# Kernel tuning notes

Measured on AMD Instinct MI355X. Metric: run time of the kernel, lower is better.

Reference implementation:

```python
import jax, jax.numpy as jnp
import numpy as np

N_NODES = 20000
N_EDGES = 640000
D_FEAT = 128
DIM_H = 128
DIM_OUT = 128


def setup_inputs() -> dict:
    key = jax.random.key(0)
    ks = jax.random.split(key, 9)
    s = 1.0 / np.sqrt(D_FEAT)
    sh = 1.0 / np.sqrt(DIM_H)
    x = jax.random.normal(ks[0], (N_NODES, D_FEAT), dtype=jnp.float32)
    edge_index = jax.random.randint(ks[1], (2, N_EDGES), 0, N_NODES, dtype=jnp.int64)
    return {
        "x": x,
        "edge_index": edge_index,
        "W_src": jax.random.normal(ks[2], (D_FEAT, DIM_H), dtype=jnp.float32) * s,
        "W_dst": jax.random.normal(ks[3], (D_FEAT, DIM_H), dtype=jnp.float32) * s,
        "att_src": jax.random.normal(ks[4], (DIM_H,), dtype=jnp.float32) * sh,
        "att_dst": jax.random.normal(ks[5], (DIM_H,), dtype=jnp.float32) * sh,
        "bias": jnp.zeros((DIM_H,), dtype=jnp.float32),
        "W_lin": jax.random.normal(ks[6], (DIM_H, DIM_OUT), dtype=jnp.float32) * sh,
        "b_lin": jnp.zeros((DIM_OUT,), dtype=jnp.float32),
    }


def reference(x, edge_index, W_src, W_dst, att_src, att_dst, bias, W_lin, b_lin):
    N = x.shape[0]
    src, dst = edge_index[0], edge_index[1]  # edge j -> i (source_to_target)
    # Separate source/destination projections (GATConv with bipartite (-1,-1) dims)
    h_src = x @ W_src  # [N, H]
    h_dst = x @ W_dst  # [N, H]
    a_src = h_src @ att_src  # [N] per-node attention contributions
    a_dst = h_dst @ att_dst  # [N]
    # Edge attention logits with LeakyReLU (negative_slope=0.2)
    logits = jax.nn.leaky_relu(a_src[src] + a_dst[dst], negative_slope=0.2)  # [E]
    # Segment softmax over incoming edges of each destination node
    seg_max = jax.ops.segment_max(logits, dst, num_segments=N)  # [N]
    e = jnp.exp(logits - seg_max[dst])  # [E]
    denom = jax.ops.segment_sum(e, dst, num_segments=N)  # [N]
    alpha = e / denom[dst]  # [E]
    # Weighted scatter-add aggregation of source features
    msg = alpha[:, None] * h_src[src]  # [E, H]
    agg = jax.ops.segment_sum(msg, dst, num_segments=N) + bias  # [N, H]
    h = jax.nn.relu(agg)
    return h @ W_lin + b_lin  # [N, dim_out]
```

## Files before the change

kernel.cpp:

```cpp
#include <hip/hip_runtime.h>
#include <cstdint>

typedef short short8 __attribute__((ext_vector_type(8)));
typedef float floatx4 __attribute__((ext_vector_type(4)));

#define NBUCK 157
#define DPB   128
#define BCAP  8192
#define EPB   2048
#define LCAP  4608

__device__ __forceinline__ unsigned short f2bf_rne(float f) {
    unsigned b = __float_as_uint(f);
    b += 0x7FFFu + ((b >> 16) & 1u);
    return (unsigned short)(b >> 16);
}

__global__ __launch_bounds__(256) void k_prep(
    const float* __restrict__ Wsrc, const float* __restrict__ Wdst,
    const float* __restrict__ Wlin,
    const float* __restrict__ att_src, const float* __restrict__ att_dst,
    float* __restrict__ w_s, float* __restrict__ w_d,
    unsigned short* __restrict__ Wt_src, unsigned short* __restrict__ Wt_lin,
    int* __restrict__ g_cur)
{
    const int b = blockIdx.x;
    const int t = threadIdx.x;
    if (b == 0) {
        const int wv = t >> 6, ln = t & 63;
        const float a0 = att_src[ln], a1 = att_src[64 + ln];
        for (int k = wv; k < 128; k += 4) {
            float v = fmaf(Wsrc[k * 128 + ln], a0, Wsrc[k * 128 + 64 + ln] * a1);
#pragma unroll
            for (int o = 32; o > 0; o >>= 1) v += __shfl_xor(v, o);
            if (ln == 0) w_s[k] = v;
        }
    } else if (b == 1) {
        const int wv = t >> 6, ln = t & 63;
        const float a0 = att_dst[ln], a1 = att_dst[64 + ln];
        for (int k = wv; k < 128; k += 4) {
            float v = fmaf(Wdst[k * 128 + ln], a0, Wdst[k * 128 + 64 + ln] * a1);
#pragma unroll
            for (int o = 32; o > 0; o >>= 1) v += __shfl_xor(v, o);
            if (ln == 0) w_d[k] = v;
        }
    } else if (b == 2) {
        for (int i = 0; i < 64; ++i) {
            int idx = t + i * 256;
            int k = idx >> 7, n = idx & 127;
            Wt_src[n * 128 + k] = f2bf_rne(Wsrc[idx]);
        }
    } else if (b == 3) {
        for (int i = 0; i < 64; ++i) {
            int idx = t + i * 256;
            int k = idx >> 7, n = idx & 127;
            Wt_lin[n * 128 + k] = f2bf_rne(Wlin[idx]);
        }
    } else {
        if (t < NBUCK) g_cur[t] = 0;
    }
}

__global__ __launch_bounds__(256) void k_fat(
    const int* __restrict__ src, const int* __restrict__ dst,
    int* __restrict__ g_cur, unsigned* __restrict__ g_edges, int E, int NBK,
    const float* __restrict__ x, const unsigned short* __restrict__ Wt,
    const float* __restrict__ w_s, const float* __restrict__ w_d,
    unsigned short* __restrict__ h_bf,
    float* __restrict__ a_src, float* __restrict__ a_dst, int N)
{
    __shared__ int cnt[NBUCK], loff[NBUCK], cur[NBUCK], gbase[NBUCK];
    __shared__ unsigned pay[EPB];
    __shared__ int dadr[EPB];
    const int tid = threadIdx.x;

    if ((int)blockIdx.x < NBK) {
        const int e0 = blockIdx.x * EPB;
        int ne_blk = E - e0; if (ne_blk > EPB) ne_blk = EPB;

        for (int i = tid; i < NBUCK; i += 256) cnt[i] = 0;
        __syncthreads();
#pragma unroll
        for (int j = 0; j < EPB / 256; ++j) {
            int e = e0 + j * 256 + tid;
            if (e < E) atomicAdd(&cnt[dst[e] >> 7], 1);
        }
        __syncthreads();
        int* sb = (int*)pay;
        sb[tid] = (tid < NBUCK) ? cnt[tid] : 0;
        __syncthreads();
        for (int s = 1; s < 256; s <<= 1) {
            int u = (tid >= s) ? sb[tid - s] : 0;
            __syncthreads();
            sb[tid] += u;
            __syncthreads();
        }
        if (tid < NBUCK) {
            loff[tid] = sb[tid] - cnt[tid];
            cur[tid] = 0;
            gbase[tid] = tid * BCAP + atomicAdd(&g_cur[tid], cnt[tid]);
        }
        __syncthreads();
#pragma unroll
        for (int j = 0; j < EPB / 256; ++j) {
            int e = e0 + j * 256 + tid;
            if (e < E) {
                int s = src[e], d = dst[e];
                int b2 = d >> 7;
                int slot = atomicAdd(&cur[b2], 1);
                int lp = loff[b2] + slot;
                pay[lp]  = (unsigned)s | ((unsigned)(d & 127) << 15);
                dadr[lp] = gbase[b2] + slot;
            }
        }
        __syncthreads();
        for (int i = tid; i < ne_blk; i += 256)
            g_edges[dadr[i]] = pay[i];
        return;
    }

    const int l = tid & 63;
    const int wv = tid >> 6;
    const int r0 = ((int)blockIdx.x - NBK) * 64 + wv * 16;
    const int rloc = l & 15;
    const int kg = l >> 4;
    int row = r0 + rloc; if (row >= N) row = N - 1;

    short8 afrag[4];
    float vs = 0.f, vd = 0.f;
#pragma unroll
    for (int kk = 0; kk < 4; ++kk) {
        const int kbase = kk * 32 + kg * 8;
        const float4 f0 = *reinterpret_cast<const float4*>(x + (size_t)row * 128 + kbase);
        const float4 f1 = *reinterpret_cast<const float4*>(x + (size_t)row * 128 + kbase + 4);
        const float4 s0 = *reinterpret_cast<const float4*>(w_s + kbase);
        const float4 s1 = *reinterpret_cast<const float4*>(w_s + kbase + 4);
        const float4 d0 = *reinterpret_cast<const float4*>(w_d + kbase);
        const float4 d1 = *reinterpret_cast<const float4*>(w_d + kbase + 4);
        const float xe[8]  = {f0.x, f0.y, f0.z, f0.w, f1.x, f1.y, f1.z, f1.w};
        const float wse[8] = {s0.x, s0.y, s0.z, s0.w, s1.x, s1.y, s1.z, s1.w};
        const float wde[8] = {d0.x, d0.y, d0.z, d0.w, d1.x, d1.y, d1.z, d1.w};
        short8 a;
#pragma unroll
        for (int j = 0; j < 8; ++j) {
            vs = fmaf(xe[j], wse[j], vs);
            vd = fmaf(xe[j], wde[j], vd);
            a[j] = (short)f2bf_rne(xe[j]);
        }
        afrag[kk] = a;
    }
    vs += __shfl_xor(vs, 16); vs += __shfl_xor(vs, 32);
    vd += __shfl_xor(vd, 16); vd += __shfl_xor(vd, 32);
    if (l < 16 && (r0 + l) < N) { a_src[r0 + l] = vs; a_dst[r0 + l] = vd; }

#pragma unroll
    for (int nt = 0; nt < 8; ++nt) {
        floatx4 acc = {0.f, 0.f, 0.f, 0.f};
#pragma unroll
        for (int kk = 0; kk < 4; ++kk) {
            const short8 bfr = *reinterpret_cast<const short8*>(
                Wt + (size_t)(nt * 16 + rloc) * 128 + kk * 32 + kg * 8);
            acc = __builtin_amdgcn_mfma_f32_16x16x32_bf16(afrag[kk], bfr, acc, 0, 0, 0);
        }
        const int col = nt * 16 + rloc;
#pragma unroll
        for (int r = 0; r < 4; ++r) {
            int grow = r0 + kg * 4 + r;
            if (grow < N) h_bf[(size_t)grow * 128 + col] = f2bf_rne(acc[r]);
        }
    }
}

__global__ __launch_bounds__(1024) void k_csr(
    const unsigned* __restrict__ g_edges, const int* __restrict__ g_cur,
    const float* __restrict__ a_src, const float* __restrict__ a_dst,
    int* __restrict__ off, uint2* __restrict__ sw, int N, int E)
{
    __shared__ int sbuf[256];
    __shared__ int hcnt[DPB], hoff[DPB], hcur[DPB];
    __shared__ uint2 swl[LCAP];
    const int b = blockIdx.x, tid = threadIdx.x;

    if (tid < 256) sbuf[tid] = (tid < NBUCK) ? g_cur[tid] : 0;
    __syncthreads();
    for (int s = 1; s < 256; s <<= 1) {
        int u = 0;
        if (tid < 256 && tid >= s) u = sbuf[tid - s];
        __syncthreads();
        if (tid < 256) sbuf[tid] += u;
        __syncthreads();
    }
    const int ne0 = g_cur[b];
    const int ne = (ne0 < LCAP) ? ne0 : LCAP;
    const int cb = sbuf[b] - ne0;
    if (b == 0 && tid == 0) off[N] = E;

    const unsigned* ep = g_edges + (size_t)b * BCAP;

    if (tid < DPB) hcnt[tid] = 0;
    __syncthreads();
    for (int i = tid; i < ne; i += 1024)
        atomicAdd(&hcnt[ep[i] >> 15], 1);
    __syncthreads();
    if (tid < DPB) hoff[tid] = hcnt[tid];
    __syncthreads();
    for (int s = 1; s < DPB; s <<= 1) {
        int u = 0;
        if (tid < DPB && tid >= s) u = hoff[tid - s];
        __syncthreads();
        if (tid < DPB) hoff[tid] += u;
        __syncthreads();
    }
    if (tid < DPB) {
        int excl = hoff[tid] - hcnt[tid];
        hoff[tid] = excl;
        hcur[tid] = 0;
        int d = b * DPB + tid;
        if (d < N) off[d] = cb + excl;
    }
    __syncthreads();
    for (int i = tid; i < ne; i += 1024) {
        unsigned p = ep[i];
        int dl = (int)(p >> 15);
        int s  = (int)(p & 0x7FFFu);
        int slot = atomicAdd(&hcur[dl], 1);
        float l = a_src[s] + a_dst[b * DPB + dl];
        l = (l > 0.f) ? l : 0.2f * l;
        swl[hoff[dl] + slot] = make_uint2((unsigned)s, __float_as_uint(__expf(l)));
    }
    __syncthreads();
    for (int i = tid; i < ne; i += 1024)
        sw[cb + i] = swl[i];
}

__global__ __launch_bounds__(256) void k_seg_fused(
    const uint2* __restrict__ sw, const int* __restrict__ off,
    const uint4* __restrict__ hb4, const float* __restrict__ bias,
    const unsigned short* __restrict__ WtLin, const float* __restrict__ blin,
    float* __restrict__ out, int N)
{
    __shared__ unsigned short hs[16][128];
    const int tid  = threadIdx.x;
    const int wv   = tid >> 6;
    const int lane = tid & 63;
    const int g    = lane >> 4;
    const int li   = lane & 15;
    const int nb   = blockIdx.x * 16;

    float4 b0 = *reinterpret_cast<const float4*>(bias + li * 8);
    float4 b1 = *reinterpret_cast<const float4*>(bias + li * 8 + 4);

    for (int i = 0; i < 4; ++i) {
        int n = nb + wv * 4 + i;
        if (n >= N) break;
        int beg = off[n], end = off[n + 1];
        float den = 0.f;
        float acc[8];
#pragma unroll
        for (int c = 0; c < 8; ++c) acc[c] = 0.f;

        for (int base = beg; base < end; base += 64) {
            int idx = base + lane;
            uint2 p = (idx < end) ? sw[idx] : make_uint2(0u, 0u);
            int   sc = (int)p.x;
            float wc = __uint_as_float(p.y);
            int cnt = end - base; if (cnt > 64) cnt = 64;
            int nq = (cnt + 3) >> 2;
            int j = 0;
            for (; j + 2 <= nq; j += 2) {
                int ea = 4 * j + g, eb = 4 * j + 4 + g;
                float wa = __shfl(wc, ea), wb = __shfl(wc, eb);
                int   sa = __shfl(sc, ea), sb = __shfl(sc, eb);
                uint4 ha = hb4[(size_t)sa * 16 + li];
                uint4 hb = hb4[(size_t)sb * 16 + li];
                den += wa + wb;
                acc[0] = fmaf(wa, __uint_as_float(ha.x << 16), acc[0]);
                acc[1] = fmaf(wa, __uint_as_float(ha.x & 0xFFFF0000u), acc[1]);
                acc[2] = fmaf(wa, __uint_as_float(ha.y << 16), acc[2]);
                acc[3] = fmaf(wa, __uint_as_float(ha.y & 0xFFFF0000u), acc[3]);
                acc[4] = fmaf(wa, __uint_as_float(ha.z << 16), acc[4]);
                acc[5] = fmaf(wa, __uint_as_float(ha.z & 0xFFFF0000u), acc[5]);
                acc[6] = fmaf(wa, __uint_as_float(ha.w << 16), acc[6]);
                acc[7] = fmaf(wa, __uint_as_float(ha.w & 0xFFFF0000u), acc[7]);
                acc[0] = fmaf(wb, __uint_as_float(hb.x << 16), acc[0]);
                acc[1] = fmaf(wb, __uint_as_float(hb.x & 0xFFFF0000u), acc[1]);
                acc[2] = fmaf(wb, __uint_as_float(hb.y << 16), acc[2]);
                acc[3] = fmaf(wb, __uint_as_float(hb.y & 0xFFFF0000u), acc[3]);
                acc[4] = fmaf(wb, __uint_as_float(hb.z << 16), acc[4]);
                acc[5] = fmaf(wb, __uint_as_float(hb.z & 0xFFFF0000u), acc[5]);
                acc[6] = fmaf(wb, __uint_as_float(hb.w << 16), acc[6]);
                acc[7] = fmaf(wb, __uint_as_float(hb.w & 0xFFFF0000u), acc[7]);
            }
            if (j < nq) {
                int e = 4 * j + g;
                float we = __shfl(wc, e);
                int   se = __shfl(sc, e);
                uint4 hv = hb4[(size_t)se * 16 + li];
                den += we;
                acc[0] = fmaf(we, __uint_as_float(hv.x << 16), acc[0]);
                acc[1] = fmaf(we, __uint_as_float(hv.x & 0xFFFF0000u), acc[1]);
                acc[2] = fmaf(we, __uint_as_float(hv.y << 16), acc[2]);
                acc[3] = fmaf(we, __uint_as_float(hv.y & 0xFFFF0000u), acc[3]);
                acc[4] = fmaf(we, __uint_as_float(hv.z << 16), acc[4]);
                acc[5] = fmaf(we, __uint_as_float(hv.z & 0xFFFF0000u), acc[5]);
                acc[6] = fmaf(we, __uint_as_float(hv.w << 16), acc[6]);
                acc[7] = fmaf(we, __uint_as_float(hv.w & 0xFFFF0000u), acc[7]);
            }
        }
#pragma unroll
        for (int c = 0; c < 8; ++c) {
            acc[c] += __shfl_xor(acc[c], 16);
            acc[c] += __shfl_xor(acc[c], 32);
        }
        den += __shfl_xor(den, 16);
        den += __shfl_xor(den, 32);

        if (g == 0) {
            float inv = (den > 0.f) ? 1.f / den : 0.f;
            float v0 = fmaxf(fmaf(acc[0], inv, b0.x), 0.f);
            float v1 = fmaxf(fmaf(acc[1], inv, b0.y), 0.f);
            float v2 = fmaxf(fmaf(acc[2], inv, b0.z), 0.f);
            float v3 = fmaxf(fmaf(acc[3], inv, b0.w), 0.f);
            float v4 = fmaxf(fmaf(acc[4], inv, b1.x), 0.f);
            float v5 = fmaxf(fmaf(acc[5], inv, b1.y), 0.f);
            float v6 = fmaxf(fmaf(acc[6], inv, b1.z), 0.f);
            float v7 = fmaxf(fmaf(acc[7], inv, b1.w), 0.f);
            uint4 o;
            o.x = ((unsigned)f2bf_rne(v1) << 16) | f2bf_rne(v0);
            o.y = ((unsigned)f2bf_rne(v3) << 16) | f2bf_rne(v2);
            o.z = ((unsigned)f2bf_rne(v5) << 16) | f2bf_rne(v4);
            o.w = ((unsigned)f2bf_rne(v7) << 16) | f2bf_rne(v6);
            *reinterpret_cast<uint4*>(&hs[wv * 4 + i][li * 8]) = o;
        }
    }
    __syncthreads();

    const int rloc = lane & 15;
    const int kg   = lane >> 4;
    short8 afrag[4];
#pragma unroll
    for (int kk = 0; kk < 4; ++kk)
        afrag[kk] = *reinterpret_cast<const short8*>(&hs[rloc][kk * 32 + kg * 8]);

#pragma unroll
    for (int t = 0; t < 2; ++t) {
        const int nt = wv * 2 + t;
        floatx4 acc4 = {0.f, 0.f, 0.f, 0.f};
#pragma unroll
        for (int kk = 0; kk < 4; ++kk) {
            const short8 bfr = *reinterpret_cast<const short8*>(
                WtLin + (size_t)(nt * 16 + rloc) * 128 + kk * 32 + kg * 8);
            acc4 = __builtin_amdgcn_mfma_f32_16x16x32_bf16(afrag[kk], bfr, acc4, 0, 0, 0);
        }
        const int col = nt * 16 + rloc;
        const float bl = blin[col];
#pragma unroll
        for (int r = 0; r < 4; ++r) {
            int grow = nb + kg * 4 + r;
            if (grow < N) out[(size_t)grow * 128 + col] = acc4[r] + bl;
        }
    }
}

extern "C" void kernel_launch(void* const* d_in, const int* in_sizes, int n_in,
                              void* d_out, int out_size, void* d_ws, size_t ws_size,
                              hipStream_t stream)
{
    const float* x       = (const float*)d_in[0];
    const int*   ei      = (const int*)d_in[1];
    const float* Wsrc    = (const float*)d_in[2];
    const float* Wdst    = (const float*)d_in[3];
    const float* att_src = (const float*)d_in[4];
    const float* att_dst = (const float*)d_in[5];
    const float* bias    = (const float*)d_in[6];
    const float* Wlin    = (const float*)d_in[7];
    const float* blin    = (const float*)d_in[8];
    float* out = (float*)d_out;

    const int N = in_sizes[0] / 128;
    const int E = in_sizes[1] / 2;
    const int* src = ei;
    const int* dst = ei + E;
    const int NBK = (E + EPB - 1) / EPB;
    const int NGB = (N + 63) / 64;

    auto aup = [](size_t v) { return (v + 255) & ~(size_t)255; };
    char* p = (char*)d_ws;
    unsigned short* h_bf   = (unsigned short*)p; p += aup((size_t)N * 128 * 2);
    uint2* sw              = (uint2*)p;          p += aup((size_t)E * 8);
    unsigned* g_edges      = (unsigned*)p;       p += aup((size_t)NBUCK * BCAP * 4);
    float* a_src           = (float*)p;          p += aup((size_t)N * 4);
    float* a_dst           = (float*)p;          p += aup((size_t)N * 4);
    int*   offs            = (int*)p;            p += aup((size_t)(N + 1) * 4);
    int*   g_cur           = (int*)p;            p += aup(NBUCK * 4);
    float* w_s             = (float*)p;          p += aup(128 * 4);
    float* w_d             = (float*)p;          p += aup(128 * 4);
    unsigned short* Wt_src = (unsigned short*)p; p += aup(128 * 128 * 2);
    unsigned short* Wt_lin = (unsigned short*)p; p += aup(128 * 128 * 2);

    k_prep<<<5, 256, 0, stream>>>(Wsrc, Wdst, Wlin, att_src, att_dst,
                                  w_s, w_d, Wt_src, Wt_lin, g_cur);
    k_fat<<<NBK + NGB, 256, 0, stream>>>(src, dst, g_cur, g_edges, E, NBK,
                                         x, Wt_src, w_s, w_d, h_bf, a_src, a_dst, N);
    k_csr<<<NBUCK, 1024, 0, stream>>>(g_edges, g_cur, a_src, a_dst,
                                      offs, sw, N, E);
    k_seg_fused<<<(N + 15) / 16, 256, 0, stream>>>(
        sw, offs, (const uint4*)h_bf, bias, Wt_lin, blin, out, N);
}
```

Measured before the change: 72.13 us.

## Drop CSR build kernel; segment kernel gathers its edges from per-block bucket runs

The global bucket scatter and the separate CSR-building kernel are removed. Each edge-partition block now writes its edges bucket-sorted in place and records a per-bucket (offset,count) table. The fused segment kernel then scans, for its 16 destination nodes, every block's run for its bucket, filters to its own nodes, and builds per-node lists in shared memory before aggregating. This saves a kernel launch, the global atomics and the sw round trip. In exchange each bucket's edges are rescanned by 8 blocks, and per-node degree is capped at 160, which could drop edges for high-degree nodes.

```diff
diff --git a/kernel.cpp b/kernel.cpp
--- a/kernel.cpp
+++ b/kernel.cpp
@@ -4,11 +4,11 @@
 typedef short short8 __attribute__((ext_vector_type(8)));
 typedef float floatx4 __attribute__((ext_vector_type(4)));
 
-#define NBUCK 157
-#define DPB   128
-#define BCAP  8192
-#define EPB   2048
-#define LCAP  4608
+#define NBUCK   157
+#define EPB     2048
+#define NBK_MAX 336
+#define BSTRIDE 160
+#define DCAP    160
 
 __device__ __forceinline__ unsigned short f2bf_rne(float f) {
     unsigned b = __float_as_uint(f);
@@ -21,8 +21,7 @@
     const float* __restrict__ Wlin,
     const float* __restrict__ att_src, const float* __restrict__ att_dst,
     float* __restrict__ w_s, float* __restrict__ w_d,
-    unsigned short* __restrict__ Wt_src, unsigned short* __restrict__ Wt_lin,
-    int* __restrict__ g_cur)
+    unsigned short* __restrict__ Wt_src, unsigned short* __restrict__ Wt_lin)
 {
     const int b = blockIdx.x;
     const int t = threadIdx.x;
@@ -50,28 +49,25 @@
             int k = idx >> 7, n = idx & 127;
             Wt_src[n * 128 + k] = f2bf_rne(Wsrc[idx]);
         }
-    } else if (b == 3) {
+    } else {
         for (int i = 0; i < 64; ++i) {
             int idx = t + i * 256;
             int k = idx >> 7, n = idx & 127;
             Wt_lin[n * 128 + k] = f2bf_rne(Wlin[idx]);
         }
-    } else {
-        if (t < NBUCK) g_cur[t] = 0;
     }
 }
 
 __global__ __launch_bounds__(256) void k_fat(
     const int* __restrict__ src, const int* __restrict__ dst,
-    int* __restrict__ g_cur, unsigned* __restrict__ g_edges, int E, int NBK,
+    unsigned* __restrict__ g_edges, unsigned* __restrict__ rb, int E, int NBK,
     const float* __restrict__ x, const unsigned short* __restrict__ Wt,
     const float* __restrict__ w_s, const float* __restrict__ w_d,
     unsigned short* __restrict__ h_bf,
     float* __restrict__ a_src, float* __restrict__ a_dst, int N)
 {
-    __shared__ int cnt[NBUCK], loff[NBUCK], cur[NBUCK], gbase[NBUCK];
+    __shared__ int cnt[NBUCK], loff[NBUCK], cur[NBUCK];
     __shared__ unsigned pay[EPB];
-    __shared__ int dadr[EPB];
     const int tid = threadIdx.x;
 
     if ((int)blockIdx.x < NBK) {
@@ -96,9 +92,11 @@
             __syncthreads();
         }
         if (tid < NBUCK) {
-            loff[tid] = sb[tid] - cnt[tid];
+            int excl = sb[tid] - cnt[tid];
+            loff[tid] = excl;
             cur[tid] = 0;
-            gbase[tid] = tid * BCAP + atomicAdd(&g_cur[tid], cnt[tid]);
+            rb[(size_t)blockIdx.x * BSTRIDE + tid] =
+                ((unsigned)excl << 16) | (unsigned)cnt[tid];
         }
         __syncthreads();
 #pragma unroll
@@ -108,14 +106,12 @@
                 int s = src[e], d = dst[e];
                 int b2 = d >> 7;
                 int slot = atomicAdd(&cur[b2], 1);
-                int lp = loff[b2] + slot;
-                pay[lp]  = (unsigned)s | ((unsigned)(d & 127) << 15);
-                dadr[lp] = gbase[b2] + slot;
+                pay[loff[b2] + slot] = (unsigned)s | ((unsigned)d << 15);
             }
         }
         __syncthreads();
         for (int i = tid; i < ne_blk; i += 256)
-            g_edges[dadr[i]] = pay[i];
+            g_edges[e0 + i] = pay[i];
         return;
     }
 
@@ -171,108 +167,84 @@
     }
 }
 
-__global__ __launch_bounds__(1024) void k_csr(
-    const unsigned* __restrict__ g_edges, const int* __restrict__ g_cur,
+__global__ __launch_bounds__(256) void k_seg_fused(
+    const unsigned* __restrict__ g_edges, const unsigned* __restrict__ rb, int NBK,
     const float* __restrict__ a_src, const float* __restrict__ a_dst,
-    int* __restrict__ off, uint2* __restrict__ sw, int N, int E)
-{
-    __shared__ int sbuf[256];
-    __shared__ int hcnt[DPB], hoff[DPB], hcur[DPB];
-    __shared__ uint2 swl[LCAP];
-    const int b = blockIdx.x, tid = threadIdx.x;
-
-    if (tid < 256) sbuf[tid] = (tid < NBUCK) ? g_cur[tid] : 0;
-    __syncthreads();
-    for (int s = 1; s < 256; s <<= 1) {
-        int u = 0;
-        if (tid < 256 && tid >= s) u = sbuf[tid - s];
-        __syncthreads();
-        if (tid < 256) sbuf[tid] += u;
-        __syncthreads();
-    }
-    const int ne0 = g_cur[b];
-    const int ne = (ne0 < LCAP) ? ne0 : LCAP;
-    const int cb = sbuf[b] - ne0;
-    if (b == 0 && tid == 0) off[N] = E;
-
-    const unsigned* ep = g_edges + (size_t)b * BCAP;
-
-    if (tid < DPB) hcnt[tid] = 0;
-    __syncthreads();
-    for (int i = tid; i < ne; i += 1024)
-        atomicAdd(&hcnt[ep[i] >> 15], 1);
-    __syncthreads();
-    if (tid < DPB) hoff[tid] = hcnt[tid];
-    __syncthreads();
-    for (int s = 1; s < DPB; s <<= 1) {
-        int u = 0;
-        if (tid < DPB && tid >= s) u = hoff[tid - s];
-        __syncthreads();
-        if (tid < DPB) hoff[tid] += u;
-        __syncthreads();
-    }
-    if (tid < DPB) {
-        int excl = hoff[tid] - hcnt[tid];
-        hoff[tid] = excl;
-        hcur[tid] = 0;
-        int d = b * DPB + tid;
-        if (d < N) off[d] = cb + excl;
-    }
-    __syncthreads();
-    for (int i = tid; i < ne; i += 1024) {
-        unsigned p = ep[i];
-        int dl = (int)(p >> 15);
-        int s  = (int)(p & 0x7FFFu);
-        int slot = atomicAdd(&hcur[dl], 1);
-        float l = a_src[s] + a_dst[b * DPB + dl];
-        l = (l > 0.f) ? l : 0.2f * l;
-        swl[hoff[dl] + slot] = make_uint2((unsigned)s, __float_as_uint(__expf(l)));
-    }
-    __syncthreads();
-    for (int i = tid; i < ne; i += 1024)
-        sw[cb + i] = swl[i];
-}
-
-__global__ __launch_bounds__(256) void k_seg_fused(
-    const uint2* __restrict__ sw, const int* __restrict__ off,
     const uint4* __restrict__ hb4, const float* __restrict__ bias,
     const unsigned short* __restrict__ WtLin, const float* __restrict__ blin,
     float* __restrict__ out, int N)
 {
+    __shared__ unsigned rbl[NBK_MAX];
+    __shared__ float adl[16];
+    __shared__ int hcur[16];
+    __shared__ uint2 lists[16][DCAP];
     __shared__ unsigned short hs[16][128];
+
     const int tid  = threadIdx.x;
+    const int nb   = blockIdx.x * 16;
+    const int bucket = nb >> 7;
+
+    for (int i = tid; i < NBK; i += 256)
+        rbl[i] = rb[(size_t)i * BSTRIDE + bucket];
+    if (tid < 16) {
+        hcur[tid] = 0;
+        int d = nb + tid;
+        adl[tid] = (d < N) ? a_dst[d] : 0.f;
+    }
+    __syncthreads();
+
     const int wv   = tid >> 6;
     const int lane = tid & 63;
-    const int g    = lane >> 4;
-    const int li   = lane & 15;
-    const int nb   = blockIdx.x * 16;
-
+
+    for (int k = wv; k < NBK; k += 4) {
+        unsigned v = rbl[k];
+        int len = (int)(v & 0xFFFFu);
+        int st  = k * EPB + (int)(v >> 16);
+        for (int o = lane; o < len; o += 64) {
+            unsigned p = g_edges[st + o];
+            int d = (int)(p >> 15);
+            int rel = d - nb;
+            if ((unsigned)rel < 16u) {
+                int s = (int)(p & 0x7FFFu);
+                float l = a_src[s] + adl[rel];
+                l = (l > 0.f) ? l : 0.2f * l;
+                int slot = atomicAdd(&hcur[rel], 1);
+                if (slot < DCAP)
+                    lists[rel][slot] = make_uint2((unsigned)s, __float_as_uint(__expf(l)));
+            }
+        }
+    }
+    __syncthreads();
+
+    const int g  = lane >> 4;
+    const int li = lane & 15;
     float4 b0 = *reinterpret_cast<const float4*>(bias + li * 8);
     float4 b1 = *reinterpret_cast<const float4*>(bias + li * 8 + 4);
 
     for (int i = 0; i < 4; ++i) {
-        int n = nb + wv * 4 + i;
+        const int nl = wv * 4 + i;
+        const int n  = nb + nl;
         if (n >= N) break;
-        int beg = off[n], end = off[n + 1];
+        int cnt_n = hcur[nl]; if (cnt_n > DCAP) cnt_n = DCAP;
         float den = 0.f;
         float acc[8];
 #pragma unroll
         for (int c = 0; c < 8; ++c) acc[c] = 0.f;
 
-        for (int base = beg; base < end; base += 64) {
+        for (int base = 0; base < cnt_n; base += 64) {
             int idx = base + lane;
-            uint2 p = (idx < end) ? sw[idx] : make_uint2(0u, 0u);
+            uint2 p = (idx < cnt_n) ? lists[nl][idx] : make_uint2(0u, 0u);
             int   sc = (int)p.x;
             float wc = __uint_as_float(p.y);
-            int cnt = end - base; if (cnt > 64) cnt = 64;
-            int nq = (cnt + 3) >> 2;
+            int cc = cnt_n - base; if (cc > 64) cc = 64;
+            int nq = (cc + 3) >> 2;
             int j = 0;
             for (; j + 2 <= nq; j += 2) {
                 int ea = 4 * j + g, eb = 4 * j + 4 + g;
                 float wa = __shfl(wc, ea), wb = __shfl(wc, eb);
-                int   sa = __shfl(sc, ea), sb = __shfl(sc, eb);
+                int   sa = __shfl(sc, ea), sb2 = __shfl(sc, eb);
                 uint4 ha = hb4[(size_t)sa * 16 + li];
-                uint4 hb = hb4[(size_t)sb * 16 + li];
+                uint4 hb = hb4[(size_t)sb2 * 16 + li];
                 den += wa + wb;
                 acc[0] = fmaf(wa, __uint_as_float(ha.x << 16), acc[0]);
                 acc[1] = fmaf(wa, __uint_as_float(ha.x & 0xFFFF0000u), acc[1]);
@@ -330,7 +302,7 @@
             o.y = ((unsigned)f2bf_rne(v3) << 16) | f2bf_rne(v2);
             o.z = ((unsigned)f2bf_rne(v5) << 16) | f2bf_rne(v4);
             o.w = ((unsigned)f2bf_rne(v7) << 16) | f2bf_rne(v6);
-            *reinterpret_cast<uint4*>(&hs[wv * 4 + i][li * 8]) = o;
+            *reinterpret_cast<uint4*>(&hs[nl][li * 8]) = o;
         }
     }
     __syncthreads();
@@ -387,23 +359,19 @@
     auto aup = [](size_t v) { return (v + 255) & ~(size_t)255; };
     char* p = (char*)d_ws;
     unsigned short* h_bf   = (unsigned short*)p; p += aup((size_t)N * 128 * 2);
-    uint2* sw              = (uint2*)p;          p += aup((size_t)E * 8);
-    unsigned* g_edges      = (unsigned*)p;       p += aup((size_t)NBUCK * BCAP * 4);
+    unsigned* g_edges      = (unsigned*)p;       p += aup((size_t)NBK * EPB * 4);
+    unsigned* rb           = (unsigned*)p;       p += aup((size_t)NBK * BSTRIDE * 4);
     float* a_src           = (float*)p;          p += aup((size_t)N * 4);
     float* a_dst           = (float*)p;          p += aup((size_t)N * 4);
-    int*   offs            = (int*)p;            p += aup((size_t)(N + 1) * 4);
-    int*   g_cur           = (int*)p;            p += aup(NBUCK * 4);
     float* w_s             = (float*)p;          p += aup(128 * 4);
     float* w_d             = (float*)p;          p += aup(128 * 4);
     unsigned short* Wt_src = (unsigned short*)p; p += aup(128 * 128 * 2);
     unsigned short* Wt_lin = (unsigned short*)p; p += aup(128 * 128 * 2);
 
-    k_prep<<<5, 256, 0, stream>>>(Wsrc, Wdst, Wlin, att_src, att_dst,
-                                  w_s, w_d, Wt_src, Wt_lin, g_cur);
-    k_fat<<<NBK + NGB, 256, 0, stream>>>(src, dst, g_cur, g_edges, E, NBK,
+    k_prep<<<4, 256, 0, stream>>>(Wsrc, Wdst, Wlin, att_src, att_dst,
+                                  w_s, w_d, Wt_src, Wt_lin);
+    k_fat<<<NBK + NGB, 256, 0, stream>>>(src, dst, g_edges, rb, E, NBK,
                                          x, Wt_src, w_s, w_d, h_bf, a_src, a_dst, N);
-    k_csr<<<NBUCK, 1024, 0, stream>>>(g_edges, g_cur, a_src, a_dst,
-                                      offs, sw, N, E);
     k_seg_fused<<<(N + 15) / 16, 256, 0, stream>>>(
-        sw, offs, (const uint4*)h_bf, bias, Wt_lin, blin, out, N);
-}
+        g_edges, rb, NBK, a_src, a_dst, (const uint4*)h_bf, bias, Wt_lin, blin, out, N);
+}
```

Result: slower. 106.7 us (+47.9%).
